# Optimization experiments

Hardware: AMD Instinct MI355X
Metric: run time of the kernel (lower is better)

The kernel has to match this reference:

```python
import jax, jax.numpy as jnp
import numpy as np

N = 4096
CIN = 128
COUT = 128
J = 2
DENSITY = 0.01  # ~40 nonzeros per Laplacian row


def _mask(k):
    m = (jax.random.uniform(k, (N, N)) < DENSITY).astype(jnp.float32)
    # Laplacians have nonzero diagonals; also guarantees no empty softmax rows
    return jnp.maximum(m, jnp.eye(N, dtype=jnp.float32))


def setup_inputs() -> dict:
    key = jax.random.key(0)
    ks = jax.random.split(key, 9)
    x = jax.random.normal(ks[0], (N, CIN), dtype=jnp.float32)
    Lup = _mask(ks[1])
    Ldown = _mask(ks[2])
    P = jax.random.normal(ks[3], (N, N), dtype=jnp.float32) / np.float32(np.sqrt(N))
    weight_irr = jax.random.normal(ks[4], (J, CIN, COUT), dtype=jnp.float32) * 0.05
    weight_sol = jax.random.normal(ks[5], (J, CIN, COUT), dtype=jnp.float32) * 0.05
    weight_har = jax.random.normal(ks[6], (CIN, COUT), dtype=jnp.float32) * 0.05
    att_irr = jax.random.normal(ks[7], (2 * J * COUT, 1), dtype=jnp.float32) * 0.05
    att_sol = jax.random.normal(ks[8], (2 * J * COUT, 1), dtype=jnp.float32) * 0.05
    return {"x": x, "Lup": Lup, "Ldown": Ldown, "P": P,
            "weight_irr": weight_irr, "weight_sol": weight_sol,
            "weight_har": weight_har, "att_irr": att_irr, "att_sol": att_sol}


def _masked_row_softmax(e, mask):
    # torch.sparse.softmax over the mask's nonzero pattern, dim=1, then to_dense
    on = mask > 0
    z = jnp.where(on, e, -jnp.inf)
    m = jnp.max(z, axis=1, keepdims=True)
    m = jnp.where(jnp.isfinite(m), m, 0.0)  # guard fully-masked rows
    p = jnp.exp(z - m)                      # exp(-inf)=0 off-pattern
    s = jnp.sum(p, axis=1, keepdims=True)
    s = jnp.where(s == 0, 1.0, s)
    return jnp.where(on, p / s, 0.0)


def _branch(x, weight, att, mask):
    j, cout = weight.shape[0], weight.shape[2]
    att_slice = j * cout
    h = jnp.einsum('ni,jio->jno', x, weight)         # [J, N, Cout]
    hf = h.reshape(-1, att_slice)                    # [N, J*Cout] (row-major, as torch)
    src = hf @ att[:att_slice]                       # [N, 1]
    dst = hf @ att[att_slice:]                       # [N, 1]
    e = jax.nn.leaky_relu(src + dst.T)               # [N, N], slope 0.01 (torch default)
    alpha = _masked_row_softmax(e, mask)             # [N, N]
    powers = [alpha]
    for _ in range(j - 1):
        powers.append(powers[-1] @ alpha)            # iterative matrix powers
    alpha_exp = jnp.stack(powers)                    # [J, N, N]
    # torch.sum with no dim: full reduction to a SCALAR (faithful to source)
    return jnp.sum(jnp.einsum('jnm,jmo->jno', alpha_exp, h))


def reference(x, Lup, Ldown, P, weight_irr, weight_sol, weight_har, att_irr, att_sol):
    z_irr = _branch(x, weight_irr, att_irr, Ldown)   # scalar
    z_sol = _branch(x, weight_sol, att_sol, Lup)     # scalar
    z_har = (P @ x) @ weight_har                     # [N, Cout]
    return z_irr + z_sol + z_har
```

## Files before the change

### kernel.cpp

```cpp
#include <hip/hip_runtime.h>

typedef __attribute__((ext_vector_type(8))) short short8b;
typedef __attribute__((ext_vector_type(4))) float f32x4;

#define NEG_SENTINEL (-1e30f)
#define GLOBAL_AS __attribute__((address_space(1)))
#define LDS_AS __attribute__((address_space(3)))

constexpr int C_OFF    = 0;
constexpr int C2_OFF   = 8192;
constexpr int SC_OFF   = 16384;
constexpr int FLAG_I   = 16390;
constexpr int ZERO_N   = 16448;
constexpr int V_OFF    = 16448;
constexpr int NP_OFF   = 19008;
constexpr int SRC_OFF  = 100928;
constexpr int RM_OFF   = 117312;
constexpr int RS_OFF   = 125504;
constexpr int NNZ_OFF  = 133696;
constexpr int CCI_OFF  = 141888;
constexpr int XBT_OFF  = 666176;
constexpr int TP_OFF   = 928320;
constexpr int AV_OFF   = 928320;

__device__ __forceinline__ unsigned short f2bf(float f) {
  unsigned int u = __float_as_uint(f);
  u += 0x7FFFu + ((u >> 16) & 1u);
  return (unsigned short)(u >> 16);
}
__device__ __forceinline__ float bf2f(unsigned short b) {
  return __uint_as_float(((unsigned int)b) << 16);
}
__device__ __forceinline__ float scrub(float v) {
  unsigned int u = __float_as_uint(v);
  return ((u & 0x7F800000u) == 0x7F800000u) ? 0.f : v;
}

__global__ __launch_bounds__(128) void k_vvec(const void* __restrict__ xin,
                                              const void* __restrict__ w_irr,
                                              const void* __restrict__ w_sol,
                                              const void* __restrict__ att_irr,
                                              const void* __restrict__ att_sol,
                                              int* __restrict__ flagp,
                                              float* __restrict__ vvec) {
  __shared__ int sdet[128];
  int t = threadIdx.x;
  unsigned int ef = (((const unsigned int*)xin)[t] >> 7) & 0xFFu;
  sdet[t] = (ef >= 100u && ef <= 150u) ? 1 : 0;
  __syncthreads();
  for (int d = 64; d > 0; d >>= 1) { if (t < d) sdet[t] += sdet[t + d]; __syncthreads(); }
  int f = (sdet[0] >= 96) ? 1 : 0;
  if (blockIdx.x == 0 && t == 0) *flagp = f;
  int bx = blockIdx.x;
  int b = bx / 10, rem = bx % 10, j = rem / 5, tt = rem % 5;
  const void* Wv = (b == 0 ? w_irr : w_sol);
  const void* Av = (b == 0 ? att_irr : att_sol);
  int i = t;
  float s = 0.f;
  if (f) {
    const unsigned short* Wr = (const unsigned short*)Wv + (size_t)j * 16384 + (size_t)i * 128;
    const unsigned short* Ar = (const unsigned short*)Av + tt * 128;
    for (int o = 0; o < 128; o += 8) {
      uint4 wq = *(const uint4*)(Wr + o);
      unsigned int ww[4] = {wq.x, wq.y, wq.z, wq.w};
      float cf[8];
      if (tt < 4) {
        uint4 aq = *(const uint4*)(Ar + o);
        unsigned int aa[4] = {aq.x, aq.y, aq.z, aq.w};
#pragma unroll
        for (int u = 0; u < 4; ++u) {
          cf[2 * u] = bf2f((unsigned short)(aa[u] & 0xFFFFu));
          cf[2 * u + 1] = bf2f((unsigned short)(aa[u] >> 16));
        }
      } else {
#pragma unroll
        for (int e = 0; e < 8; ++e) cf[e] = 1.0f;
      }
#pragma unroll
      for (int u = 0; u < 4; ++u) {
        s += bf2f((unsigned short)(ww[u] & 0xFFFFu)) * cf[2 * u];
        s += bf2f((unsigned short)(ww[u] >> 16)) * cf[2 * u + 1];
      }
    }
  } else {
    const float* Wr = (const float*)Wv + (size_t)j * 16384 + (size_t)i * 128;
    const float* Ar = (const float*)Av + tt * 128;
    for (int o = 0; o < 128; o += 4) {
      float4 wq = *(const float4*)(Wr + o);
      float4 aq = {1.f, 1.f, 1.f, 1.f};
      if (tt < 4) aq = *(const float4*)(Ar + o);
      s += wq.x * aq.x + wq.y * aq.y + wq.z * aq.z + wq.w * aq.w;
    }
  }
  vvec[bx * 128 + i] = s;
}

__global__ __launch_bounds__(256) void k_prep(const void* __restrict__ xin,
                                              const int* __restrict__ flag,
                                              const float* __restrict__ vvec,
                                              unsigned short* __restrict__ xbT,
                                              float* __restrict__ np,
                                              float* __restrict__ srcdst) {
  __shared__ __align__(16) float ldsx[64 * 130];
  __shared__ __align__(16) float ldsv[2560];
  __shared__ float ldsp[4 * 1280];
  __shared__ float npl[1280];
  int f = *flag;
  int t = threadIdx.x, nb = blockIdx.x * 64;
  for (int q = 0; q < 16; ++q) {
    int idx = q * 256 + t;
    int row = idx >> 6, cp = idx & 63;
    float vx, vy;
    if (f) {
      unsigned int u = ((const unsigned int*)xin)[(size_t)(nb + row) * 64 + cp];
      vx = bf2f((unsigned short)(u & 0xFFFFu));
      vy = bf2f((unsigned short)(u >> 16));
    } else {
      float2 v = ((const float2*)xin)[(size_t)(nb + row) * 64 + cp];
      vx = v.x; vy = v.y;
    }
    ldsx[row * 130 + cp * 2] = vx;
    ldsx[row * 130 + cp * 2 + 1] = vy;
  }
  for (int q = 0; q < 10; ++q) { int idx = q * 256 + t; ldsv[idx] = vvec[idx]; }
  __syncthreads();
  for (int q = 0; q < 32; ++q) {
    int idx = q * 256 + t;
    int c = idx >> 6, n = idx & 63;
    xbT[(size_t)c * 4096 + nb + n] = f2bf(ldsx[n * 130 + c]);
  }
  int row = t & 63, qq = t >> 6, i0 = qq * 32;
  float acc[20];
#pragma unroll
  for (int k = 0; k < 20; ++k) acc[k] = 0.f;
  for (int i = i0; i < i0 + 32; i += 2) {
    float2 xv = *(const float2*)&ldsx[row * 130 + i];
#pragma unroll
    for (int k = 0; k < 20; ++k) {
      float2 vk = *(const float2*)&ldsv[k * 128 + i];
      acc[k] += xv.x * vk.x + xv.y * vk.y;
    }
  }
#pragma unroll
  for (int k = 0; k < 20; ++k) ldsp[qq * 1280 + row * 20 + k] = acc[k];
  __syncthreads();
  for (int rep = 0; rep < 5; ++rep) {
    int idx = rep * 256 + t;
    int k = idx >> 6, rr = idx & 63;
    float s = ldsp[rr * 20 + k] + ldsp[1280 + rr * 20 + k] +
              ldsp[2560 + rr * 20 + k] + ldsp[3840 + rr * 20 + k];
    npl[k * 64 + rr] = s;
    np[(size_t)k * 4096 + nb + rr] = s;
  }
  __syncthreads();
  {
    int b = t >> 7, j = (t >> 6) & 1, kind = (t >> 5) & 1, q = t & 31;
    int bl = q * 2;
    int r = j * 2048 + (nb >> 1) + q;
    int kidx = b * 10 + j * 5 + kind * 2;
    float val = npl[kidx * 64 + bl] + npl[(kidx + 1) * 64 + bl + 1];
    srcdst[b * 8192 + kind * 4096 + r] = val;
  }
}

__device__ __forceinline__ int col_of(int f, int l, int bit) {
  if (f) return ((bit >> 3) * 512) + l * 8 + (bit & 7);
  return ((bit >> 5) * 2048) + (((bit >> 2) & 7) * 256) + l * 4 + (bit & 3);
}

__global__ __launch_bounds__(256) void k_scan(const void* __restrict__ Ldown,
                                              const void* __restrict__ Lup,
                                              float* __restrict__ ws) {
  __shared__ __align__(16) unsigned short rows[4][4096];
  int b = blockIdx.y, t = threadIdx.x;
  int wid = t >> 6, l = t & 63;
  int r = blockIdx.x * 4 + wid;
  int f = ((const int*)ws)[FLAG_I];
  unsigned short* cci = (unsigned short*)(ws + CCI_OFF) + (size_t)(b * 4096 + r) * 128;
  unsigned long long hm = 0ULL;
  if (f) {
    const unsigned short* gsrc = (const unsigned short*)(b ? Lup : Ldown) +
                                 (size_t)r * 4096 + l * 8;
    unsigned short* ldst = &rows[wid][0];
#pragma unroll
    for (int j = 0; j < 8; ++j) {
      __builtin_amdgcn_global_load_lds(
          (const GLOBAL_AS unsigned int*)(gsrc + j * 512),
          (LDS_AS unsigned int*)(ldst + j * 512), 16, 0, 0);
    }
    asm volatile("s_waitcnt vmcnt(0)" ::: "memory");
    __builtin_amdgcn_sched_barrier(0);
#pragma unroll
    for (int it = 0; it < 8; ++it) {
      uint4 cs = *(const uint4*)&rows[wid][it * 512 + l * 8];
      unsigned int wv[4] = {cs.x, cs.y, cs.z, cs.w};
#pragma unroll
      for (int u = 0; u < 4; ++u) {
        hm |= ((unsigned long long)((wv[u] & 0xFFFFu) != 0u)) << (it * 8 + u * 2);
        hm |= ((unsigned long long)((wv[u] >> 16) != 0u)) << (it * 8 + u * 2 + 1);
      }
    }
  } else {
    const uint4* rp = (const uint4*)((const float*)(b ? Lup : Ldown) +
                                     (size_t)r * 4096) + l;
#pragma unroll
    for (int p = 0; p < 2; ++p) {
      uint4 cs[8];
#pragma unroll
      for (int it = 0; it < 8; ++it) cs[it] = rp[(p * 8 + it) * 64];
#pragma unroll
      for (int it = 0; it < 8; ++it) {
        unsigned int wv[4] = {cs[it].x, cs[it].y, cs[it].z, cs[it].w};
#pragma unroll
        for (int u = 0; u < 4; ++u)
          hm |= ((unsigned long long)(wv[u] != 0u)) << (p * 32 + it * 4 + u);
      }
    }
  }
  int cnt = __popcll(hm);
  int pre = cnt;
  for (int d = 1; d < 64; d <<= 1) {
    int o = __shfl_up(pre, d);
    if (l >= d) pre += o;
  }
  int base = pre - cnt;
  int nz = __shfl(pre, 63);
  if (l == 0) ((int*)ws)[NNZ_OFF + b * 4096 + r] = min(nz, 128);
  const float* srcp = ws + SRC_OFF + b * 8192;
  const float* dstp = srcp + 4096;
  float srcr = srcp[r];
  float mx = NEG_SENTINEL, sm = 0.f;
  unsigned long long mm = hm;
  while (mm) {
    int bit = __builtin_ctzll(mm); mm &= mm - 1;
    int m = col_of(f, l, bit);
    float e = srcr + dstp[m];
    e = (e >= 0.f) ? e : 0.01f * e;
    if (e > mx) { sm = sm * __expf(mx - e) + 1.f; mx = e; }
    else        { sm += __expf(e - mx); }
  }
  for (int d = 1; d < 64; d <<= 1) {
    float om = __shfl_xor(mx, d);
    float os = __shfl_xor(sm, d);
    float M = fmaxf(mx, om);
    sm = sm * __expf(mx - M) + os * __expf(om - M);
    mx = M;
  }
  float inv = 1.0f / sm;
  float* av = ws + AV_OFF + (size_t)(b * 4096 + r) * 128;
  int slot = base;
  mm = hm;
  while (mm) {
    int bit = __builtin_ctzll(mm); mm &= mm - 1;
    int m = col_of(f, l, bit);
    float e = srcr + dstp[m];
    e = (e >= 0.f) ? e : 0.01f * e;
    float p = __expf(e - mx) * inv;
    if (slot < 128) { cci[slot] = (unsigned short)m; av[slot] = p; }
    ++slot;
    atomicAdd(&ws[C_OFF + b * 4096 + m], p);
  }
}

__global__ __launch_bounds__(256) void k_c2(float* __restrict__ ws) {
  int b = blockIdx.y, t = threadIdx.x;
  int wid = t >> 6, l = t & 63;
  int r = blockIdx.x * 4 + wid;
  const unsigned short* cci =
      (const unsigned short*)(ws + CCI_OFF) + (size_t)(b * 4096 + r) * 128;
  const float* av = ws + AV_OFF + (size_t)(b * 4096 + r) * 128;
  int m0 = cci[l];
  int m1 = cci[l + 64];
  float a0 = av[l];
  float a1 = av[l + 64];
  float cr = ws[C_OFF + b * 4096 + r];
  int nz = ((const int*)ws)[NNZ_OFF + b * 4096 + r];
  if (l < nz)
    atomicAdd(&ws[C2_OFF + b * 4096 + m0], cr * a0);
  if (l + 64 < nz)
    atomicAdd(&ws[C2_OFF + b * 4096 + m1], cr * a1);
}

__global__ __launch_bounds__(256) void k_scalar(float* __restrict__ ws) {
  int b = blockIdx.x, t = threadIdx.x;
  const float* cb  = ws + C_OFF  + b * 4096;
  const float* c2b = ws + C2_OFF + b * 4096;
  const float* hr0 = ws + NP_OFF + (b * 10 + 4) * 4096;
  const float* hr1 = ws + NP_OFF + (b * 10 + 9) * 4096;
  double acc = 0.0;
  for (int m = t; m < 4096; m += 256)
    acc += (double)scrub(cb[m]) * (double)scrub(hr0[m]) +
           (double)scrub(c2b[m]) * (double)scrub(hr1[m]);
  __shared__ double sd[256];
  sd[t] = acc;
  __syncthreads();
  for (int s = 128; s > 0; s >>= 1) { if (t < s) sd[t] += sd[t + s]; __syncthreads(); }
  if (t == 0) atomicAdd(&ws[SC_OFF], (float)sd[0]);
}

__global__ __launch_bounds__(256) void k_gemm1(const void* __restrict__ P,
                                               const unsigned short* __restrict__ xbT,
                                               const int* __restrict__ flag,
                                               float* __restrict__ TP) {
  __shared__ __align__(16) unsigned short a_lds[64 * 40];
  __shared__ __align__(16) unsigned short b_lds[128 * 40];
  int f = *flag;
  const int mt = blockIdx.x & 63, ks = blockIdx.x >> 6;
  const int mb = mt * 64;
  const int t = threadIdx.x;
  const int w = t >> 6, l = t & 63, quad = l >> 4, lr = l & 15;
  f32x4 acc[8] = {};
  const int arow = t >> 2, akq = (t & 3) << 3;
  const int bn = t >> 1, bh = (t & 1) << 4;
  const int k0 = ks * 512;
  uint4 aU, bU0, bU1;
#define LOADT(IT)                                                              \
  {                                                                            \
    const int kb = k0 + (IT) * 32;                                             \
    if (f) {                                                                   \
      aU = *(const uint4*)((const unsigned short*)P +                          \
                           (size_t)(mb + arow) * 4096 + kb + akq);             \
    } else {                                                                   \
      const float* pa = (const float*)P + (size_t)(mb + arow) * 4096 + kb + akq; \
      float4 f0 = *(const float4*)pa;                                          \
      float4 f1 = *(const float4*)(pa + 4);                                    \
      unsigned short u[8] = {f2bf(f0.x), f2bf(f0.y), f2bf(f0.z), f2bf(f0.w),   \
                             f2bf(f1.x), f2bf(f1.y), f2bf(f1.z), f2bf(f1.w)};  \
      aU = *(const uint4*)u;                                                   \
    }                                                                          \
    const unsigned short* src = xbT + (size_t)bn * 4096 + kb + bh;             \
    bU0 = *(const uint4*)src;                                                  \
    bU1 = *(const uint4*)(src + 8);                                            \
  }
  LOADT(0);
  for (int it = 0; it < 16; ++it) {
    *(uint4*)&a_lds[arow * 40 + akq] = aU;
    *(uint4*)&b_lds[bn * 40 + bh] = bU0;
    *(uint4*)&b_lds[bn * 40 + bh + 8] = bU1;
    __syncthreads();
    if (it < 15) LOADT(it + 1);
    short8b af = *(short8b*)&a_lds[(w * 16 + lr) * 40 + quad * 8];
#pragma unroll
    for (int nt = 0; nt < 8; ++nt) {
      short8b bf = *(short8b*)&b_lds[(nt * 16 + lr) * 40 + quad * 8];
      acc[nt] = __builtin_amdgcn_mfma_f32_16x16x32_bf16(af, bf, acc[nt], 0, 0, 0);
    }
    if (it < 15) __syncthreads();
  }
#undef LOADT
  float* Tp = TP + (size_t)ks * 524288;
#pragma unroll
  for (int nt = 0; nt < 8; ++nt)
#pragma unroll
    for (int rr = 0; rr < 4; ++rr) {
      int row = mb + w * 16 + quad * 4 + rr;
      int col = nt * 16 + lr;
      Tp[(size_t)row * 128 + col] = acc[nt][rr];
    }
}

__global__ __launch_bounds__(256) void k_gemm2(const float* __restrict__ TP,
                                               const void* __restrict__ W,
                                               const float* __restrict__ ws,
                                               void* __restrict__ outv) {
  __shared__ float tl[16 * 128];
  int f = ((const int*)ws)[FLAG_I];
  int t = threadIdx.x;
  int rb = blockIdx.x * 16;
  for (int q = 0; q < 2; ++q) {
    int vi = q * 256 + t;
    size_t base = (size_t)rb * 128 + (size_t)vi * 4;
    float4 s = {0.f, 0.f, 0.f, 0.f};
#pragma unroll
    for (int p = 0; p < 8; ++p) {
      float4 v = *(const float4*)&TP[(size_t)p * 524288 + base];
      s.x += v.x; s.y += v.y; s.z += v.z; s.w += v.w;
    }
    *(float4*)&tl[vi * 4] = s;
  }
  __syncthreads();
  int col = t & 127, rg = t >> 7;
  int r0 = rg * 8;
  float acc[8] = {};
  for (int k = 0; k < 128; k += 4) {
    float w0, w1, w2, w3;
    if (f) {
      const unsigned short* W16 = (const unsigned short*)W;
      w0 = bf2f(W16[(k + 0) * 128 + col]); w1 = bf2f(W16[(k + 1) * 128 + col]);
      w2 = bf2f(W16[(k + 2) * 128 + col]); w3 = bf2f(W16[(k + 3) * 128 + col]);
    } else {
      const float* W32 = (const float*)W;
      w0 = W32[(k + 0) * 128 + col]; w1 = W32[(k + 1) * 128 + col];
      w2 = W32[(k + 2) * 128 + col]; w3 = W32[(k + 3) * 128 + col];
    }
#pragma unroll
    for (int rr = 0; rr < 8; ++rr) {
      float4 tv = *(const float4*)&tl[(r0 + rr) * 128 + k];
      acc[rr] += tv.x * w0 + tv.y * w1 + tv.z * w2 + tv.w * w3;
    }
  }
  float s = scrub(ws[SC_OFF]);
#pragma unroll
  for (int rr = 0; rr < 8; ++rr) {
    size_t oi = (size_t)(rb + r0 + rr) * 128 + col;
    float v = s + acc[rr];
    if (f) ((unsigned short*)outv)[oi] = f2bf(v);
    else   ((float*)outv)[oi] = v;
  }
}

extern "C" void kernel_launch(void* const* d_in, const int* in_sizes, int n_in,
                              void* d_out, int out_size, void* d_ws, size_t ws_size,
                              hipStream_t stream) {
  const void* x       = d_in[0];
  const void* Lup     = d_in[1];
  const void* Ldown   = d_in[2];
  const void* P       = d_in[3];
  const void* w_irr   = d_in[4];
  const void* w_sol   = d_in[5];
  const void* w_har   = d_in[6];
  const void* att_irr = d_in[7];
  const void* att_sol = d_in[8];
  float* ws = (float*)d_ws;

  hipMemsetAsync(d_ws, 0, (size_t)ZERO_N * sizeof(float), stream);
  k_vvec  <<<20, 128, 0, stream>>>(x, w_irr, w_sol, att_irr, att_sol,
                                   (int*)ws + FLAG_I, ws + V_OFF);
  k_prep  <<<64, 256, 0, stream>>>(x, (int*)ws + FLAG_I, ws + V_OFF,
                                   (unsigned short*)(ws + XBT_OFF), ws + NP_OFF,
                                   ws + SRC_OFF);
  k_scan  <<<dim3(1024, 2), 256, 0, stream>>>(Ldown, Lup, ws);
  k_c2    <<<dim3(1024, 2), 256, 0, stream>>>(ws);
  k_scalar<<<2, 256, 0, stream>>>(ws);
  k_gemm1 <<<512, 256, 0, stream>>>(P, (const unsigned short*)(ws + XBT_OFF),
                                    (int*)ws + FLAG_I, ws + TP_OFF);
  k_gemm2 <<<256, 256, 0, stream>>>(ws + TP_OFF, w_har, ws, d_out);
}
```

Baseline: 312.7 us.

## Split mask scan into bitmask-building kernel and compact bitmask-based softmax scan

Adds a k_mask kernel that reads both Laplacians once and packs nonzero flags into a bitmask workspace. k_scan now reads 64 bits per lane from this bitmask instead of streaming whole dense rows, and computes the column index as l*64+bit. The goal is a fully parallel, coalesced pass over the dense masks, separate from the latency-bound per-row softmax work, and a simpler scan kernel. The cost is an extra launch plus a bitmask write and read in global memory.

```diff
diff --git a/kernel.cpp b/kernel.cpp
--- a/kernel.cpp
+++ b/kernel.cpp
@@ -4,8 +4,6 @@
 typedef __attribute__((ext_vector_type(4))) float f32x4;
 
 #define NEG_SENTINEL (-1e30f)
-#define GLOBAL_AS __attribute__((address_space(1)))
-#define LDS_AS __attribute__((address_space(3)))
 
 constexpr int C_OFF    = 0;
 constexpr int C2_OFF   = 8192;
@@ -15,13 +13,12 @@
 constexpr int V_OFF    = 16448;
 constexpr int NP_OFF   = 19008;
 constexpr int SRC_OFF  = 100928;
-constexpr int RM_OFF   = 117312;
-constexpr int RS_OFF   = 125504;
 constexpr int NNZ_OFF  = 133696;
 constexpr int CCI_OFF  = 141888;
 constexpr int XBT_OFF  = 666176;
 constexpr int TP_OFF   = 928320;
 constexpr int AV_OFF   = 928320;
+constexpr int BM_OFF   = 1976896;
 
 __device__ __forceinline__ unsigned short f2bf(float f) {
   unsigned int u = __float_as_uint(f);
@@ -163,60 +160,62 @@
   }
 }
 
-__device__ __forceinline__ int col_of(int f, int l, int bit) {
-  if (f) return ((bit >> 3) * 512) + l * 8 + (bit & 7);
-  return ((bit >> 5) * 2048) + (((bit >> 2) & 7) * 256) + l * 4 + (bit & 3);
-}
-
-__global__ __launch_bounds__(256) void k_scan(const void* __restrict__ Ldown,
+__global__ __launch_bounds__(256) void k_mask(const void* __restrict__ Ldown,
                                               const void* __restrict__ Lup,
                                               float* __restrict__ ws) {
-  __shared__ __align__(16) unsigned short rows[4][4096];
+  int f = ((const int*)ws)[FLAG_I];
+  int t = threadIdx.x;
+  if (f) {
+    int gw = blockIdx.x * 4 + (t >> 6), l = t & 63;
+    int b = gw >> 13, wv = gw & 8191;
+    const unsigned short* src = (const unsigned short*)(b ? Lup : Ldown) +
+                                (size_t)wv * 2048;
+    unsigned char* outb = (unsigned char*)(ws + BM_OFF) +
+                          (size_t)b * 2097152 + wv * 256;
+    uint4 c[4];
+#pragma unroll
+    for (int j = 0; j < 4; ++j)
+      c[j] = *(const uint4*)(src + j * 512 + l * 8);
+#pragma unroll
+    for (int j = 0; j < 4; ++j) {
+      unsigned int w4[4] = {c[j].x, c[j].y, c[j].z, c[j].w};
+      unsigned int by = 0;
+#pragma unroll
+      for (int u = 0; u < 4; ++u) {
+        by |= ((w4[u] & 0xFFFFu) != 0u ? 1u : 0u) << (u * 2);
+        by |= ((w4[u] >> 16) != 0u ? 1u : 0u) << (u * 2 + 1);
+      }
+      outb[j * 64 + l] = (unsigned char)by;
+    }
+  } else {
+    int w = blockIdx.x * 256 + t;
+    int b = w >> 19, widx = w & 524287;
+    const float* src = (const float*)(b ? Lup : Ldown) + (size_t)widx * 32;
+    unsigned int bits = 0;
+#pragma unroll
+    for (int q = 0; q < 8; ++q) {
+      uint4 c = *(const uint4*)(src + q * 4);
+      bits |= (c.x != 0u ? 1u : 0u) << (q * 4 + 0);
+      bits |= (c.y != 0u ? 1u : 0u) << (q * 4 + 1);
+      bits |= (c.z != 0u ? 1u : 0u) << (q * 4 + 2);
+      bits |= (c.w != 0u ? 1u : 0u) << (q * 4 + 3);
+    }
+    ((unsigned int*)(ws + BM_OFF))[w] = bits;
+  }
+}
+
+__global__ __launch_bounds__(256) void k_scan(float* __restrict__ ws) {
   int b = blockIdx.y, t = threadIdx.x;
   int wid = t >> 6, l = t & 63;
   int r = blockIdx.x * 4 + wid;
-  int f = ((const int*)ws)[FLAG_I];
+  const unsigned int* bm = (const unsigned int*)(ws + BM_OFF) +
+                           (size_t)b * 524288 + r * 128;
+  const float* srcp = ws + SRC_OFF + b * 8192;
+  const float* dstp = srcp + 4096;
+  float srcr = srcp[r];
+  uint2 v = *(const uint2*)(bm + l * 2);
+  unsigned long long hm = ((unsigned long long)v.y << 32) | v.x;
   unsigned short* cci = (unsigned short*)(ws + CCI_OFF) + (size_t)(b * 4096 + r) * 128;
-  unsigned long long hm = 0ULL;
-  if (f) {
-    const unsigned short* gsrc = (const unsigned short*)(b ? Lup : Ldown) +
-                                 (size_t)r * 4096 + l * 8;
-    unsigned short* ldst = &rows[wid][0];
-#pragma unroll
-    for (int j = 0; j < 8; ++j) {
-      __builtin_amdgcn_global_load_lds(
-          (const GLOBAL_AS unsigned int*)(gsrc + j * 512),
-          (LDS_AS unsigned int*)(ldst + j * 512), 16, 0, 0);
-    }
-    asm volatile("s_waitcnt vmcnt(0)" ::: "memory");
-    __builtin_amdgcn_sched_barrier(0);
-#pragma unroll
-    for (int it = 0; it < 8; ++it) {
-      uint4 cs = *(const uint4*)&rows[wid][it * 512 + l * 8];
-      unsigned int wv[4] = {cs.x, cs.y, cs.z, cs.w};
-#pragma unroll
-      for (int u = 0; u < 4; ++u) {
-        hm |= ((unsigned long long)((wv[u] & 0xFFFFu) != 0u)) << (it * 8 + u * 2);
-        hm |= ((unsigned long long)((wv[u] >> 16) != 0u)) << (it * 8 + u * 2 + 1);
-      }
-    }
-  } else {
-    const uint4* rp = (const uint4*)((const float*)(b ? Lup : Ldown) +
-                                     (size_t)r * 4096) + l;
-#pragma unroll
-    for (int p = 0; p < 2; ++p) {
-      uint4 cs[8];
-#pragma unroll
-      for (int it = 0; it < 8; ++it) cs[it] = rp[(p * 8 + it) * 64];
-#pragma unroll
-      for (int it = 0; it < 8; ++it) {
-        unsigned int wv[4] = {cs[it].x, cs[it].y, cs[it].z, cs[it].w};
-#pragma unroll
-        for (int u = 0; u < 4; ++u)
-          hm |= ((unsigned long long)(wv[u] != 0u)) << (p * 32 + it * 4 + u);
-      }
-    }
-  }
   int cnt = __popcll(hm);
   int pre = cnt;
   for (int d = 1; d < 64; d <<= 1) {
@@ -226,14 +225,11 @@
   int base = pre - cnt;
   int nz = __shfl(pre, 63);
   if (l == 0) ((int*)ws)[NNZ_OFF + b * 4096 + r] = min(nz, 128);
-  const float* srcp = ws + SRC_OFF + b * 8192;
-  const float* dstp = srcp + 4096;
-  float srcr = srcp[r];
   float mx = NEG_SENTINEL, sm = 0.f;
   unsigned long long mm = hm;
   while (mm) {
     int bit = __builtin_ctzll(mm); mm &= mm - 1;
-    int m = col_of(f, l, bit);
+    int m = l * 64 + bit;
     float e = srcr + dstp[m];
     e = (e >= 0.f) ? e : 0.01f * e;
     if (e > mx) { sm = sm * __expf(mx - e) + 1.f; mx = e; }
@@ -252,7 +248,7 @@
   mm = hm;
   while (mm) {
     int bit = __builtin_ctzll(mm); mm &= mm - 1;
-    int m = col_of(f, l, bit);
+    int m = l * 64 + bit;
     float e = srcr + dstp[m];
     e = (e >= 0.f) ? e : 0.01f * e;
     float p = __expf(e - mx) * inv;
@@ -429,7 +425,8 @@
   k_prep  <<<64, 256, 0, stream>>>(x, (int*)ws + FLAG_I, ws + V_OFF,
                                    (unsigned short*)(ws + XBT_OFF), ws + NP_OFF,
                                    ws + SRC_OFF);
-  k_scan  <<<dim3(1024, 2), 256, 0, stream>>>(Ldown, Lup, ws);
+  k_mask  <<<4096, 256, 0, stream>>>(Ldown, Lup, ws);
+  k_scan  <<<dim3(1024, 2), 256, 0, stream>>>(ws);
   k_c2    <<<dim3(1024, 2), 256, 0, stream>>>(ws);
   k_scalar<<<2, 256, 0, stream>>>(ws);
   k_gemm1 <<<512, 256, 0, stream>>>(P, (const unsigned short*)(ws + XBT_OFF),
```

Result: slower. 324.9 us (+3.9%).
